# Kernel optimization log

Hardware: AMD Instinct MI355X
Metric: run time of the kernel (lower is better)

The kernel has to match this reference:

```python
import jax, jax.numpy as jnp
import numpy as np

B, D, L, T, K = 16, 256, 256, 1000, 3
DW, DC = 4, 2  # dim_w, dim_c
CH = 8         # ConvSwishBlock out channels (10 = 1 start + 1 end + 8)


def swish(x):
    return x * jax.nn.sigmoid(x)


def setup_inputs() -> dict:
    key = jax.random.key(0)
    ks = jax.random.split(key, 12)
    # durations ~ U[1,6] per phone -> sum ~ 3.5*L ~ 896 <= T
    durations = 1.0 + 5.0 * jax.random.uniform(ks[0], (B, L), dtype=jnp.float32)
    phoneme = jax.random.normal(ks[1], (B, D, L), dtype=jnp.float32)
    # True = padded phone position
    phone_len = L - (jnp.arange(B) % 4) * 16
    phoneme_mask = (jnp.arange(L)[None, :] >= phone_len[:, None])[:, None, :]
    durations = jnp.where(phoneme_mask[:, 0, :], 0.0, durations)
    s = 0.02
    p = {
        'proj_w_W': s * jax.random.normal(ks[2], (D, D)), 'proj_w_b': jnp.zeros((D,)),
        'conv_w_W': s * jax.random.normal(ks[3], (CH, D, K)), 'conv_w_b': jnp.zeros((CH,)),
        'mlp_w_W': s * jax.random.normal(ks[4], (2 + CH, DW)), 'mlp_w_b': jnp.zeros((DW,)),
        'lin_w_W': s * jax.random.normal(ks[5], (D * DW, D)), 'lin_w_b': jnp.zeros((D,)),
        'proj_c_W': s * jax.random.normal(ks[6], (D, D)), 'proj_c_b': jnp.zeros((D,)),
        'conv_c_W': s * jax.random.normal(ks[7], (CH, D, K)), 'conv_c_b': jnp.zeros((CH,)),
        'mlp_c_W': s * jax.random.normal(ks[8], (2 + CH, DC)), 'mlp_c_b': jnp.zeros((DC,)),
        'lin_c_W': s * jax.random.normal(ks[9], (DW * DC, D)), 'lin_c_b': jnp.zeros((D,)),
    }
    return {'durations': durations, 'phoneme': phoneme, 'phoneme_mask': phoneme_mask, **p}


def _conv_branch(x, phone_pad, projW, projb, convW, convb):
    # x: (B, D, L). 1x1 conv projection, then K-wide 'same' conv to CH channels, swish, mask.
    x = jnp.einsum('od,bdl->bol', projW, x) + projb[None, :, None]
    h = jax.lax.conv_general_dilated(x, convW, (1,), 'SAME',
                                     dimension_numbers=('NCH', 'OIH', 'NCH'))
    h = swish(h + convb[None, :, None])
    h = jnp.where(phone_pad[:, None, :], 0.0, h)
    return h.transpose(0, 2, 1)  # (B, L, CH)


def _forward(durations, phoneme, phoneme_mask,
             proj_w_W, proj_w_b, conv_w_W, conv_w_b, mlp_w_W, mlp_w_b, lin_w_W, lin_w_b,
             proj_c_W, proj_c_b, conv_c_W, conv_c_b, mlp_c_W, mlp_c_b, lin_c_W, lin_c_b):
    phone_pad = phoneme_mask[:, 0, :]                       # (B, L) True = pad
    frame_len = jnp.clip(jnp.round(jnp.sum(durations, -1)), 0, T).astype(jnp.int32)
    frame_pad = jnp.arange(T)[None, :] >= frame_len[:, None]  # (B, T) True = pad
    attn_pad = frame_pad[:, :, None] | phone_pad[:, None, :]  # (B, T, L)

    sd = jnp.cumsum(durations, -1)                          # (B, L) cumulative end times
    sk = sd - durations                                     # (B, L) start times
    t = jnp.arange(1, T + 1, dtype=durations.dtype)
    S = jnp.where(attn_pad, 0.0, t[None, :, None] - sk[:, None, :])                    # (B,T,L)
    E = jnp.where(attn_pad, 0.0, jnp.broadcast_to(sd[:, None, :], attn_pad.shape)
                  - sk[:, None, :])                                                    # (B,T,L)

    # W branch: per-(frame, phone) attention weights over phones
    h_w = _conv_branch(phoneme, phone_pad, proj_w_W, proj_w_b, conv_w_W, conv_w_b)     # (B,L,CH)
    feat_w = jnp.concatenate(
        [S[..., None], E[..., None], jnp.broadcast_to(h_w[:, None], (B, T, L, CH))], -1)
    w = swish(feat_w @ mlp_w_W + mlp_w_b)                   # (B, T, L, DW)
    w = jnp.where(phone_pad[:, None, :, None], -jnp.inf, w)
    w = jax.nn.softmax(w, axis=2)                           # softmax over phones
    w = jnp.where(frame_pad[:, :, None, None], 0.0, w)

    # C branch: auxiliary per-(frame, phone) context
    h_c = _conv_branch(phoneme, phone_pad, proj_c_W, proj_c_b, conv_c_W, conv_c_b)
    feat_c = jnp.concatenate(
        [S[..., None], E[..., None], jnp.broadcast_to(h_c[:, None], (B, T, L, CH))], -1)
    c = swish(feat_c @ mlp_c_W + mlp_c_b)                   # (B, T, L, DC)

    # combine: wh = einsum over phones with phoneme features, wc with c matrix
    wh = jnp.einsum('btnq,bnh->btqh', w, phoneme.transpose(0, 2, 1))  # (B,T,DW,D)
    wh = wh.reshape(B, T, DW * D) @ lin_w_W + lin_w_b                 # (B,T,D)
    wc = jnp.einsum('btnq,btnp->btqp', w, c)                          # (B,T,DW,DC)
    wc = wc.reshape(B, T, DW * DC) @ lin_c_W + lin_c_b                # (B,T,D)
    return wh + wc


def reference(durations, phoneme, phoneme_mask,
              proj_w_W, proj_w_b, conv_w_W, conv_w_b, mlp_w_W, mlp_w_b, lin_w_W, lin_w_b,
              proj_c_W, proj_c_b, conv_c_W, conv_c_b, mlp_c_W, mlp_c_b, lin_c_W, lin_c_b):
    return _forward(durations, phoneme, phoneme_mask,
                    proj_w_W, proj_w_b, conv_w_W, conv_w_b, mlp_w_W, mlp_w_b, lin_w_W, lin_w_b,
                    proj_c_W, proj_c_b, conv_c_W, conv_c_b, mlp_c_W, mlp_c_b, lin_c_W, lin_c_b)
```

## Files before the change

### kernel.cpp

```cpp
#include <hip/hip_runtime.h>


typedef short v8s __attribute__((ext_vector_type(8)));
typedef _Float16 v8h __attribute__((ext_vector_type(8)));
typedef float f4 __attribute__((ext_vector_type(4)));

__device__ __forceinline__ float bf2f(unsigned short h) {
  return __uint_as_float(((unsigned int)h) << 16);
}
__device__ __forceinline__ unsigned short f2bf(float f) {
  unsigned int u = __float_as_uint(f);
  u = (u + 0x7FFFu + ((u >> 16) & 1u)) >> 16;
  return (unsigned short)u;
}
__device__ __forceinline__ float swishf(float x) {
  return x * __builtin_amdgcn_rcpf(1.f + __expf(-x));
}

__global__ __launch_bounds__(256) void k_prep(
    const float* __restrict__ dur, const float* __restrict__ ph,
    const float* __restrict__ liWw,
    const float* __restrict__ cvWw, const float* __restrict__ pjWw,
    const float* __restrict__ pjbw,
    const float* __restrict__ cvWc, const float* __restrict__ pjWc,
    const float* __restrict__ pjbc,
    float* __restrict__ sk, int* __restrict__ frame_len,
    unsigned short* __restrict__ Mb, float* __restrict__ bK,
    unsigned short* __restrict__ LWT, unsigned short* __restrict__ phT) {
  __shared__ float sm[32 * 33];
  int blk = blockIdx.x, tid = threadIdx.x;
  if (blk < 16) {
    int b = blk, l = tid;
    float d = dur[b * 256 + l];
    sm[l] = d;
    __syncthreads();
    for (int off = 1; off < 256; off <<= 1) {
      float v = (l >= off) ? sm[l - off] : 0.f;
      __syncthreads();
      sm[l] += v;
      __syncthreads();
    }
    sk[b * 256 + l] = sm[l] - d;
    if (l == 255) {
      int fl = (int)rintf(sm[255]);
      frame_len[b] = min(max(fl, 0), 1000);
    }
  } else if (blk < 64) {
    int x = blk - 16;
    int br = x / 24, ck = x % 24;
    int ch = ck / 3, k = ck % 3;
    const float* convW = br ? cvWc : cvWw;
    const float* projW = br ? pjWc : pjWw;
    const float* projb = br ? pjbc : pjbw;
    int d = tid;
    float a0 = 0.f, a1 = 0.f, a2 = 0.f, a3 = 0.f;
    for (int o = 0; o < 256; o += 4) {
      a0 += convW[ch * 768 + (o + 0) * 3 + k] * projW[(o + 0) * 256 + d];
      a1 += convW[ch * 768 + (o + 1) * 3 + k] * projW[(o + 1) * 256 + d];
      a2 += convW[ch * 768 + (o + 2) * 3 + k] * projW[(o + 2) * 256 + d];
      a3 += convW[ch * 768 + (o + 3) * 3 + k] * projW[(o + 3) * 256 + d];
    }
    Mb[(br * 24 + ck) * 256 + d] = f2bf((a0 + a1) + (a2 + a3));
    if (tid < 64) {
      float pb = 0.f;
      for (int o = tid; o < 256; o += 64)
        pb += convW[ch * 768 + o * 3 + k] * projb[o];
#pragma unroll
      for (int off = 1; off < 64; off <<= 1) pb += __shfl_xor(pb, off);
      if (tid == 0) bK[br * 24 + ck] = pb;
    }
  } else if (blk < 320) {
    int idx = blk - 64;
    int kt = idx & 31, ot = idx >> 5;
    int tx = tid & 31, ty = tid >> 5;
#pragma unroll
    for (int r = 0; r < 4; r++) {
      int row = ty + r * 8;
      sm[row * 33 + tx] = liWw[(size_t)(kt * 32 + row) * 256 + ot * 32 + tx];
    }
    __syncthreads();
#pragma unroll
    for (int r = 0; r < 4; r++) {
      int row = ty + r * 8;
      LWT[(size_t)(ot * 32 + row) * 1024 + kt * 32 + tx] =
          f2bf(sm[tx * 33 + row]);
    }
  } else {
    int idx = blk - 320;
    int ht = idx & 7, lt = (idx >> 3) & 7, b = idx >> 6;
    int tx = tid & 31, ty = tid >> 5;
#pragma unroll
    for (int r = 0; r < 4; r++) {
      int row = ty + r * 8;
      sm[row * 33 + tx] =
          ph[(size_t)b * 65536 + (size_t)(ht * 32 + row) * 256 + lt * 32 + tx];
    }
    __syncthreads();
#pragma unroll
    for (int r = 0; r < 4; r++) {
      int row = ty + r * 8;
      phT[(size_t)b * 65536 + (size_t)(lt * 32 + row) * 256 + ht * 32 + tx] =
          f2bf(sm[tx * 33 + row]);
    }
  }
}

__global__ __launch_bounds__(256) void k_convG(
    const unsigned short* __restrict__ phT, const unsigned short* __restrict__ Mb,
    const float* __restrict__ bK, const float* __restrict__ cvbw,
    const float* __restrict__ cvbc, const float* __restrict__ dur,
    const float* __restrict__ sk, const float* __restrict__ mlpWw,
    const float* __restrict__ mlpbw, const float* __restrict__ mlpWc,
    const float* __restrict__ mlpbc, const unsigned short* __restrict__ LWT,
    float* __restrict__ Lbw, float* __restrict__ Laux,
    float* __restrict__ maxAb, _Float16* __restrict__ G) {
  __shared__ __align__(16) float C[256 * 49];
  __shared__ float redm[4][4];
  int blk = blockIdx.x;
  int tid = threadIdx.x, wave = tid >> 6, lane = tid & 63;
  int quad = lane >> 4, col = lane & 15;
  if (blk < 16) {
    int b = blk;
    int l0 = wave * 64;
    const unsigned short* Ab = phT + (size_t)b * 65536;
    f4 acc[4][3] = {};
#pragma unroll
    for (int k0 = 0; k0 < 256; k0 += 32) {
      v8s af[4], bf[3];
#pragma unroll
      for (int lt = 0; lt < 4; lt++)
        af[lt] = *(const v8s*)(Ab + (size_t)(l0 + lt * 16 + col) * 256 + k0 + quad * 8);
#pragma unroll
      for (int ct = 0; ct < 3; ct++)
        bf[ct] = *(const v8s*)(Mb + (size_t)(ct * 16 + col) * 256 + k0 + quad * 8);
#pragma unroll
      for (int lt = 0; lt < 4; lt++)
#pragma unroll
        for (int ct = 0; ct < 3; ct++)
          acc[lt][ct] = __builtin_amdgcn_mfma_f32_16x16x32_bf16(af[lt], bf[ct],
                                                                acc[lt][ct], 0, 0, 0);
    }
#pragma unroll
    for (int lt = 0; lt < 4; lt++)
#pragma unroll
      for (int ct = 0; ct < 3; ct++)
#pragma unroll
        for (int r = 0; r < 4; r++)
          C[(l0 + lt * 16 + quad * 4 + r) * 49 + ct * 16 + col] = acc[lt][ct][r];
    __syncthreads();
    int l = tid;
    float dv = dur[b * 256 + l];
    bool vld = (dv != 0.f);
    float hv[2][8];
#pragma unroll
    for (int br = 0; br < 2; br++) {
      const float* convb = br ? cvbc : cvbw;
#pragma unroll
      for (int ch = 0; ch < 8; ch++) {
        int ck = br * 24 + ch * 3;
        float v = convb[ch] + bK[ck + 1] + C[l * 49 + ck + 1];
        if (l > 0) v += bK[ck + 0] + C[(l - 1) * 49 + ck + 0];
        if (l < 255) v += bK[ck + 2] + C[(l + 1) * 49 + ck + 2];
        hv[br][ch] = vld ? swishf(v) : 0.f;
      }
    }
    float skl = sk[b * 256 + l];
    float A[4];
#pragma unroll
    for (int q = 0; q < 4; q++) {
      float a = mlpbw[q] + dv * mlpWw[4 + q] - skl * mlpWw[q];
#pragma unroll
      for (int ch = 0; ch < 8; ch++) a += hv[0][ch] * mlpWw[(2 + ch) * 4 + q];
      A[q] = vld ? a : -1e30f;
    }
    float bb0 = mlpbc[0] + dv * mlpWc[2] - skl * mlpWc[0];
    float bb1 = mlpbc[1] + dv * mlpWc[3] - skl * mlpWc[1];
#pragma unroll
    for (int ch = 0; ch < 8; ch++) {
      bb0 += hv[1][ch] * mlpWc[(2 + ch) * 2 + 0];
      bb1 += hv[1][ch] * mlpWc[(2 + ch) * 2 + 1];
    }
    float4 Av = {A[0], A[1], A[2], A[3]};
    ((float4*)Lbw)[b * 256 + l] = Av;
    float4 Xv = {bb0, bb1, vld ? 1.f : 0.f, 0.f};
    ((float4*)Laux)[b * 256 + l] = Xv;
    float m0 = A[0], m1 = A[1], m2 = A[2], m3 = A[3];
#pragma unroll
    for (int off = 1; off < 64; off <<= 1) {
      m0 = fmaxf(m0, __shfl_xor(m0, off));
      m1 = fmaxf(m1, __shfl_xor(m1, off));
      m2 = fmaxf(m2, __shfl_xor(m2, off));
      m3 = fmaxf(m3, __shfl_xor(m3, off));
    }
    if (lane == 0) {
      redm[wave][0] = m0;
      redm[wave][1] = m1;
      redm[wave][2] = m2;
      redm[wave][3] = m3;
    }
    __syncthreads();
    if (tid < 4)
      maxAb[b * 4 + tid] = fmaxf(fmaxf(redm[0][tid], redm[1][tid]),
                                 fmaxf(redm[2][tid], redm[3][tid]));
  } else {
    int idx = blk - 16;
    int b = idx >> 4;
    int sub = idx & 15;
    int q = sub >> 2, quadr = sub & 3;
    int mo = (quadr >> 1) * 128, nl = (quadr & 1) * 128;
    int wm = (wave & 1) * 64, wn = (wave >> 1) * 64;
    const unsigned short* Ag = LWT + (size_t)q * 256;
    const unsigned short* Bg = phT + (size_t)b * 65536;
    f4 acc[4][4] = {};
#pragma unroll
    for (int k0 = 0; k0 < 256; k0 += 32) {
      v8s af[4], bf[4];
#pragma unroll
      for (int mt = 0; mt < 4; mt++)
        af[mt] = *(const v8s*)(Ag + (size_t)(mo + wm + mt * 16 + col) * 1024 +
                               k0 + quad * 8);
#pragma unroll
      for (int nt = 0; nt < 4; nt++)
        bf[nt] = *(const v8s*)(Bg + (size_t)(nl + wn + nt * 16 + col) * 256 +
                               k0 + quad * 8);
#pragma unroll
      for (int mt = 0; mt < 4; mt++)
#pragma unroll
        for (int nt = 0; nt < 4; nt++)
          acc[mt][nt] = __builtin_amdgcn_mfma_f32_16x16x32_bf16(af[mt], bf[nt],
                                                                acc[mt][nt], 0, 0, 0);
    }
    _Float16* Gb = G + (size_t)b * 262144 + q * 256;
#pragma unroll
    for (int mt = 0; mt < 4; mt++)
#pragma unroll
      for (int r = 0; r < 4; r++) {
        int orow = mo + wm + mt * 16 + quad * 4 + r;
#pragma unroll
        for (int nt = 0; nt < 4; nt++) {
          int lcol = nl + wn + nt * 16 + col;
          Gb[(size_t)orow * 1024 + lcol] = (_Float16)acc[mt][nt][r];
        }
      }
  }
}

__global__ __launch_bounds__(256) void k_fuse(
    const float* __restrict__ Lbw, const float* __restrict__ Laux,
    const float* __restrict__ maxAb, const int* __restrict__ frame_len,
    const float* __restrict__ mlpWw, const float* __restrict__ mlpWc,
    const _Float16* __restrict__ G, const float* __restrict__ lwb,
    const float* __restrict__ lcb, const float* __restrict__ LC,
    float* __restrict__ out) {
  __shared__ __align__(16) _Float16 Asm[32 * 512];
  __shared__ __align__(16) float4 Lb4[264];
  __shared__ __align__(16) float4 Lx4[264];
  __shared__ float bias_s[256];
  __shared__ float lcs[8][256];
  __shared__ float wcs[32][8];

  int idx = blockIdx.x;
  int b = (idx & 7) * 2 + ((idx >> 3) & 1);
  int t0 = (idx >> 4) * 32;
  int tid = threadIdx.x, wave = tid >> 6, lane = tid & 63;
  int quad = lane >> 4, col = lane & 15;

  {
    float4 av = ((const float4*)Lbw)[b * 256 + tid];
    float4 xv = ((const float4*)Laux)[b * 256 + tid];
    int li = tid + (tid >> 5);
    Lb4[li] = av;
    Lx4[li] = xv;
    bias_s[tid] = lwb[tid] + lcb[tid];
#pragma unroll
    for (int i = 0; i < 8; i++) lcs[i][tid] = LC[i * 256 + tid];
  }
  int fl = frame_len[b];
  float4 mx4 = ((const float4*)maxAb)[b];
  float mw0 = mlpWw[0], mw1 = mlpWw[1], mw2 = mlpWw[2], mw3 = mlpWw[3];
  float mc0 = mlpWc[0], mc1 = mlpWc[1];

  int r_loc = lane >> 3, l_grp = lane & 7;
  int row = wave * 8 + r_loc;
  int t = t0 + row;
  bool live = (t < fl);
  float tp1 = (float)(t + 1);
  int rsw = row & 7;
  int asw = col & 7;
  int wn = wave * 64;
  f4 acc[2][4] = {};

  __syncthreads();

#pragma unroll
  for (int p = 0; p < 2; ++p) {
    if (p) __syncthreads();
    float mq0 = p ? mw2 : mw0;
    float mq1 = p ? mw3 : mw1;
    float mxa = p ? mx4.z : mx4.x;
    float mxb = p ? mx4.w : mx4.y;
    float m0 = live ? fmaxf(mxa + tp1 * mq0, 0.f) : 1e30f;
    float m1 = live ? fmaxf(mxb + tp1 * mq1, 0.f) : 1e30f;
    float s0 = 0.f, s1 = 0.f, p00 = 0.f, p01 = 0.f, p10 = 0.f, p11 = 0.f;
    v8h e0[4], e1[4];
#pragma unroll
    for (int j = 0; j < 32; ++j) {
      int l = l_grp * 32 + j;
      int li = l + (l >> 5);
      float4 A4 = Lb4[li];
      float4 ax = Lx4[li];
      float cp0 = swishf(ax.x + tp1 * mc0);
      float cp1 = swishf(ax.y + tp1 * mc1);
      float Aq0 = p ? A4.z : A4.x;
      float Aq1 = p ? A4.w : A4.y;
      float ee0 = __expf(swishf(Aq0 + tp1 * mq0) - m0) * ax.z;
      float ee1 = __expf(swishf(Aq1 + tp1 * mq1) - m1) * ax.z;
      e0[j >> 3][j & 7] = (_Float16)ee0;
      e1[j >> 3][j & 7] = (_Float16)ee1;
      s0 += ee0;
      s1 += ee1;
      p00 += ee0 * cp0;
      p01 += ee0 * cp1;
      p10 += ee1 * cp0;
      p11 += ee1 * cp1;
    }
#pragma unroll
    for (int off = 1; off < 8; off <<= 1) {
      s0 += __shfl_xor(s0, off);
      s1 += __shfl_xor(s1, off);
      p00 += __shfl_xor(p00, off);
      p01 += __shfl_xor(p01, off);
      p10 += __shfl_xor(p10, off);
      p11 += __shfl_xor(p11, off);
    }
    float iv0 = live ? __builtin_amdgcn_rcpf(s0) : 0.f;
    float iv1 = live ? __builtin_amdgcn_rcpf(s1) : 0.f;
    if (l_grp == 0) {
      wcs[row][p * 4 + 0] = p00 * iv0;
      wcs[row][p * 4 + 1] = p01 * iv0;
      wcs[row][p * 4 + 2] = p10 * iv1;
      wcs[row][p * 4 + 3] = p11 * iv1;
    }
    _Float16 h0 = (_Float16)iv0, h1 = (_Float16)iv1;
#pragma unroll
    for (int c = 0; c < 4; ++c) {
      int sl0 = (l_grp * 4 + c) ^ rsw;
      int sl1 = 32 + ((l_grp * 4 + c) ^ rsw);
      *(v8h*)&Asm[(row * 64 + sl0) * 8] = e0[c] * h0;
      *(v8h*)&Asm[(row * 64 + sl1) * 8] = e1[c] * h1;
    }
    __syncthreads();
    const _Float16* Gp = G + (size_t)b * 262144 + p * 512;
#pragma unroll 2
    for (int k0 = 0; k0 < 512; k0 += 32) {
      int slk = (k0 >> 3) + quad;
      v8h af0 = *(const v8h*)&Asm[(col * 64 + (slk ^ asw)) * 8];
      v8h af1 = *(const v8h*)&Asm[((16 + col) * 64 + (slk ^ asw)) * 8];
      v8h bf[4];
#pragma unroll
      for (int nt = 0; nt < 4; ++nt)
        bf[nt] =
            *(const v8h*)(Gp + (size_t)(wn + nt * 16 + col) * 1024 + k0 + quad * 8);
#pragma unroll
      for (int nt = 0; nt < 4; ++nt) {
        acc[0][nt] =
            __builtin_amdgcn_mfma_f32_16x16x32_f16(af0, bf[nt], acc[0][nt], 0, 0, 0);
        acc[1][nt] =
            __builtin_amdgcn_mfma_f32_16x16x32_f16(af1, bf[nt], acc[1][nt], 0, 0, 0);
      }
    }
  }
#pragma unroll
  for (int mt = 0; mt < 2; ++mt)
#pragma unroll
    for (int r = 0; r < 4; ++r) {
      int lrow = mt * 16 + quad * 4 + r;
      int trow = t0 + lrow;
      if (trow < 1000) {
        float4 wa = *(const float4*)&wcs[lrow][0];
        float4 wb = *(const float4*)&wcs[lrow][4];
        float wcl[8] = {wa.x, wa.y, wa.z, wa.w, wb.x, wb.y, wb.z, wb.w};
#pragma unroll
        for (int nt = 0; nt < 4; ++nt) {
          int oc = wn + nt * 16 + col;
          float v = acc[mt][nt][r] + bias_s[oc];
#pragma unroll
          for (int jj = 0; jj < 8; ++jj) v = fmaf(wcl[jj], lcs[jj][oc], v);
          out[((size_t)(b * 1000 + trow)) * 256 + oc] = v;
        }
      }
    }
}

extern "C" void kernel_launch(void* const* d_in, const int* in_sizes, int n_in,
                              void* d_out, int out_size, void* d_ws, size_t ws_size,
                              hipStream_t stream) {
  const float* dur  = (const float*)d_in[0];
  const float* ph   = (const float*)d_in[1];
  const float* pjWw = (const float*)d_in[3];
  const float* pjbw = (const float*)d_in[4];
  const float* cvWw = (const float*)d_in[5];
  const float* cvbw = (const float*)d_in[6];
  const float* mlWw = (const float*)d_in[7];
  const float* mlbw = (const float*)d_in[8];
  const float* liWw = (const float*)d_in[9];
  const float* libw = (const float*)d_in[10];
  const float* pjWc = (const float*)d_in[11];
  const float* pjbc = (const float*)d_in[12];
  const float* cvWc = (const float*)d_in[13];
  const float* cvbc = (const float*)d_in[14];
  const float* mlWc = (const float*)d_in[15];
  const float* mlbc = (const float*)d_in[16];
  const float* liWc = (const float*)d_in[17];
  const float* libc = (const float*)d_in[18];
  float* out = (float*)d_out;

  float* f = (float*)d_ws;
  size_t o = 0;
  float* sk = f + o;            o += 4096;
  int* fl = (int*)(f + o);      o += 16;
  float* bK = f + o;            o += 64;
  unsigned short* Mb = (unsigned short*)(f + o); o += 6144;
  float* Lbw = f + o;           o += 16384;
  float* Laux = f + o;          o += 16384;
  float* mxA = f + o;           o += 64;
  _Float16* G = (_Float16*)(f + o);              o += 2097152;
  unsigned short* phT = (unsigned short*)(f + o); o += 524288;
  unsigned short* LWT = (unsigned short*)(f + o); o += 131072;

  k_prep<<<1344, 256, 0, stream>>>(dur, ph, liWw, cvWw, pjWw, pjbw, cvWc, pjWc,
                                   pjbc, sk, fl, Mb, bK, LWT, phT);
  k_convG<<<272, 256, 0, stream>>>(phT, Mb, bK, cvbw, cvbc, dur, sk, mlWw,
                                   mlbw, mlWc, mlbc, LWT, Lbw, Laux, mxA, G);
  k_fuse<<<512, 256, 0, stream>>>(Lbw, Laux, mxA, fl, mlWw, mlWc, G, libw,
                                  libc, liWc, out);
}
```

Before: 175.6 us.

## Double threads per fuse block, split convG tiles finer, skip dead frame tiles

The G-building GEMM in k_convG now uses 64-wide column tiles, which doubles its grid to 528 blocks and halves per-wave accumulators. k_fuse moves to 512 threads per block. Each row is split across 16 lanes instead of 8, the c-branch swish values are computed once instead of per pass, and MFMA priority is raised during the GEMM loop. Blocks whose whole time tile lies beyond the frame length now just write the bias and return, skipping the softmax and GEMM. The trade-offs are more LDS padding and register pressure per thread, and normalisation now uses fp16-rounded exponentials with an exact divide.

```diff
diff --git a/kernel.cpp b/kernel.cpp
--- a/kernel.cpp
+++ b/kernel.cpp
@@ -204,29 +204,29 @@
                                  fmaxf(redm[2][tid], redm[3][tid]));
   } else {
     int idx = blk - 16;
-    int b = idx >> 4;
-    int sub = idx & 15;
-    int q = sub >> 2, quadr = sub & 3;
-    int mo = (quadr >> 1) * 128, nl = (quadr & 1) * 128;
-    int wm = (wave & 1) * 64, wn = (wave >> 1) * 64;
+    int b = idx >> 5;
+    int sub = idx & 31;
+    int q = sub >> 3, rem = sub & 7;
+    int mo = (rem >> 2) * 128, nl = (rem & 3) * 64;
+    int wm = (wave & 1) * 64, wn = (wave >> 1) * 32;
     const unsigned short* Ag = LWT + (size_t)q * 256;
     const unsigned short* Bg = phT + (size_t)b * 65536;
-    f4 acc[4][4] = {};
+    f4 acc[4][2] = {};
 #pragma unroll
     for (int k0 = 0; k0 < 256; k0 += 32) {
-      v8s af[4], bf[4];
+      v8s af[4], bf[2];
 #pragma unroll
       for (int mt = 0; mt < 4; mt++)
         af[mt] = *(const v8s*)(Ag + (size_t)(mo + wm + mt * 16 + col) * 1024 +
                                k0 + quad * 8);
 #pragma unroll
-      for (int nt = 0; nt < 4; nt++)
+      for (int nt = 0; nt < 2; nt++)
         bf[nt] = *(const v8s*)(Bg + (size_t)(nl + wn + nt * 16 + col) * 256 +
                                k0 + quad * 8);
 #pragma unroll
       for (int mt = 0; mt < 4; mt++)
 #pragma unroll
-        for (int nt = 0; nt < 4; nt++)
+        for (int nt = 0; nt < 2; nt++)
           acc[mt][nt] = __builtin_amdgcn_mfma_f32_16x16x32_bf16(af[mt], bf[nt],
                                                                 acc[mt][nt], 0, 0, 0);
     }
@@ -237,7 +237,7 @@
       for (int r = 0; r < 4; r++) {
         int orow = mo + wm + mt * 16 + quad * 4 + r;
 #pragma unroll
-        for (int nt = 0; nt < 4; nt++) {
+        for (int nt = 0; nt < 2; nt++) {
           int lcol = nl + wn + nt * 16 + col;
           Gb[(size_t)orow * 1024 + lcol] = (_Float16)acc[mt][nt][r];
         }
@@ -245,7 +245,7 @@
   }
 }
 
-__global__ __launch_bounds__(256) void k_fuse(
+__global__ __launch_bounds__(512, 4) void k_fuse(
     const float* __restrict__ Lbw, const float* __restrict__ Laux,
     const float* __restrict__ maxAb, const int* __restrict__ frame_len,
     const float* __restrict__ mlpWw, const float* __restrict__ mlpWc,
@@ -253,8 +253,8 @@
     const float* __restrict__ lcb, const float* __restrict__ LC,
     float* __restrict__ out) {
   __shared__ __align__(16) _Float16 Asm[32 * 512];
-  __shared__ __align__(16) float4 Lb4[264];
-  __shared__ __align__(16) float4 Lx4[264];
+  __shared__ __align__(16) float4 Lb4[272];
+  __shared__ __align__(16) float4 Lx4[272];
   __shared__ float bias_s[256];
   __shared__ float lcs[8][256];
   __shared__ float wcs[32][8];
@@ -265,32 +265,52 @@
   int tid = threadIdx.x, wave = tid >> 6, lane = tid & 63;
   int quad = lane >> 4, col = lane & 15;
 
-  {
+  int fl = frame_len[b];
+  if (t0 >= fl) {
+    int o = tid & 255;
+    float v = lwb[o] + lcb[o];
+    for (int r = tid >> 8; r < 32; r += 2) {
+      int t = t0 + r;
+      if (t < 1000) out[((size_t)(b * 1000 + t)) * 256 + o] = v;
+    }
+    return;
+  }
+
+  if (tid < 256) {
     float4 av = ((const float4*)Lbw)[b * 256 + tid];
     float4 xv = ((const float4*)Laux)[b * 256 + tid];
-    int li = tid + (tid >> 5);
+    int li = tid + (tid >> 4);
     Lb4[li] = av;
     Lx4[li] = xv;
     bias_s[tid] = lwb[tid] + lcb[tid];
-#pragma unroll
-    for (int i = 0; i < 8; i++) lcs[i][tid] = LC[i * 256 + tid];
-  }
-  int fl = frame_len[b];
+  }
+  for (int i = tid; i < 2048; i += 512) lcs[i >> 8][i & 255] = LC[i];
+
   float4 mx4 = ((const float4*)maxAb)[b];
   float mw0 = mlpWw[0], mw1 = mlpWw[1], mw2 = mlpWw[2], mw3 = mlpWw[3];
   float mc0 = mlpWc[0], mc1 = mlpWc[1];
 
-  int r_loc = lane >> 3, l_grp = lane & 7;
-  int row = wave * 8 + r_loc;
+  int l_grp = lane & 15;
+  int row = wave * 4 + (lane >> 4);
   int t = t0 + row;
   bool live = (t < fl);
   float tp1 = (float)(t + 1);
   int rsw = row & 7;
   int asw = col & 7;
-  int wn = wave * 64;
-  f4 acc[2][4] = {};
+  int wn = wave * 32;
+  f4 acc[2][2] = {};
 
   __syncthreads();
+
+  float cpa[16], cpb[16];
+#pragma unroll
+  for (int j = 0; j < 16; ++j) {
+    int l = l_grp * 16 + j;
+    int li = l + (l >> 4);
+    float4 ax = Lx4[li];
+    cpa[j] = swishf(ax.x + tp1 * mc0);
+    cpb[j] = swishf(ax.y + tp1 * mc1);
+  }
 
 #pragma unroll
   for (int p = 0; p < 2; ++p) {
@@ -302,30 +322,29 @@
     float m0 = live ? fmaxf(mxa + tp1 * mq0, 0.f) : 1e30f;
     float m1 = live ? fmaxf(mxb + tp1 * mq1, 0.f) : 1e30f;
     float s0 = 0.f, s1 = 0.f, p00 = 0.f, p01 = 0.f, p10 = 0.f, p11 = 0.f;
-    v8h e0[4], e1[4];
-#pragma unroll
-    for (int j = 0; j < 32; ++j) {
-      int l = l_grp * 32 + j;
-      int li = l + (l >> 5);
+    v8h e0[2], e1[2];
+#pragma unroll
+    for (int j = 0; j < 16; ++j) {
+      int l = l_grp * 16 + j;
+      int li = l + (l >> 4);
       float4 A4 = Lb4[li];
-      float4 ax = Lx4[li];
-      float cp0 = swishf(ax.x + tp1 * mc0);
-      float cp1 = swishf(ax.y + tp1 * mc1);
+      float zz = ((const float*)&Lx4[li])[2];
       float Aq0 = p ? A4.z : A4.x;
       float Aq1 = p ? A4.w : A4.y;
-      float ee0 = __expf(swishf(Aq0 + tp1 * mq0) - m0) * ax.z;
-      float ee1 = __expf(swishf(Aq1 + tp1 * mq1) - m1) * ax.z;
-      e0[j >> 3][j & 7] = (_Float16)ee0;
-      e1[j >> 3][j & 7] = (_Float16)ee1;
-      s0 += ee0;
-      s1 += ee1;
-      p00 += ee0 * cp0;
-      p01 += ee0 * cp1;
-      p10 += ee1 * cp0;
-      p11 += ee1 * cp1;
-    }
-#pragma unroll
-    for (int off = 1; off < 8; off <<= 1) {
+      _Float16 eh0 = (_Float16)(__expf(swishf(Aq0 + tp1 * mq0) - m0) * zz);
+      _Float16 eh1 = (_Float16)(__expf(swishf(Aq1 + tp1 * mq1) - m1) * zz);
+      e0[j >> 3][j & 7] = eh0;
+      e1[j >> 3][j & 7] = eh1;
+      float f0 = (float)eh0, f1 = (float)eh1;
+      s0 += f0;
+      s1 += f1;
+      p00 += f0 * cpa[j];
+      p01 += f0 * cpb[j];
+      p10 += f1 * cpa[j];
+      p11 += f1 * cpb[j];
+    }
+#pragma unroll
+    for (int off = 1; off < 16; off <<= 1) {
       s0 += __shfl_xor(s0, off);
       s1 += __shfl_xor(s1, off);
       p00 += __shfl_xor(p00, off);
@@ -333,42 +352,48 @@
       p10 += __shfl_xor(p10, off);
       p11 += __shfl_xor(p11, off);
     }
-    float iv0 = live ? __builtin_amdgcn_rcpf(s0) : 0.f;
-    float iv1 = live ? __builtin_amdgcn_rcpf(s1) : 0.f;
+    float iv0 = live ? 1.0f / s0 : 0.f;
+    float iv1 = live ? 1.0f / s1 : 0.f;
     if (l_grp == 0) {
       wcs[row][p * 4 + 0] = p00 * iv0;
       wcs[row][p * 4 + 1] = p01 * iv0;
       wcs[row][p * 4 + 2] = p10 * iv1;
       wcs[row][p * 4 + 3] = p11 * iv1;
     }
-    _Float16 h0 = (_Float16)iv0, h1 = (_Float16)iv1;
-#pragma unroll
-    for (int c = 0; c < 4; ++c) {
-      int sl0 = (l_grp * 4 + c) ^ rsw;
-      int sl1 = 32 + ((l_grp * 4 + c) ^ rsw);
-      *(v8h*)&Asm[(row * 64 + sl0) * 8] = e0[c] * h0;
-      *(v8h*)&Asm[(row * 64 + sl1) * 8] = e1[c] * h1;
+#pragma unroll
+    for (int c = 0; c < 2; ++c) {
+      int sl = (l_grp * 2 + c) ^ rsw;
+      v8h w0, w1;
+#pragma unroll
+      for (int k = 0; k < 8; ++k) {
+        w0[k] = (_Float16)((float)e0[c][k] * iv0);
+        w1[k] = (_Float16)((float)e1[c][k] * iv1);
+      }
+      *(v8h*)&Asm[(row * 64 + sl) * 8] = w0;
+      *(v8h*)&Asm[(row * 64 + 32 + sl) * 8] = w1;
     }
     __syncthreads();
     const _Float16* Gp = G + (size_t)b * 262144 + p * 512;
+    __builtin_amdgcn_s_setprio(1);
 #pragma unroll 2
     for (int k0 = 0; k0 < 512; k0 += 32) {
       int slk = (k0 >> 3) + quad;
-      v8h af0 = *(const v8h*)&Asm[(col * 64 + (slk ^ asw)) * 8];
-      v8h af1 = *(const v8h*)&Asm[((16 + col) * 64 + (slk ^ asw)) * 8];
-      v8h bf[4];
-#pragma unroll
-      for (int nt = 0; nt < 4; ++nt)
+      v8h af[2], bf[2];
+#pragma unroll
+      for (int mt = 0; mt < 2; ++mt)
+        af[mt] = *(const v8h*)&Asm[((mt * 16 + col) * 64 + (slk ^ asw)) * 8];
+#pragma unroll
+      for (int nt = 0; nt < 2; ++nt)
         bf[nt] =
             *(const v8h*)(Gp + (size_t)(wn + nt * 16 + col) * 1024 + k0 + quad * 8);
 #pragma unroll
-      for (int nt = 0; nt < 4; ++nt) {
-        acc[0][nt] =
-            __builtin_amdgcn_mfma_f32_16x16x32_f16(af0, bf[nt], acc[0][nt], 0, 0, 0);
-        acc[1][nt] =
-            __builtin_amdgcn_mfma_f32_16x16x32_f16(af1, bf[nt], acc[1][nt], 0, 0, 0);
-      }
-    }
+      for (int mt = 0; mt < 2; ++mt)
+#pragma unroll
+        for (int nt = 0; nt < 2; ++nt)
+          acc[mt][nt] = __builtin_amdgcn_mfma_f32_16x16x32_f16(af[mt], bf[nt],
+                                                               acc[mt][nt], 0, 0, 0);
+    }
+    __builtin_amdgcn_s_setprio(0);
   }
 #pragma unroll
   for (int mt = 0; mt < 2; ++mt)
@@ -381,7 +406,7 @@
         float4 wb = *(const float4*)&wcs[lrow][4];
         float wcl[8] = {wa.x, wa.y, wa.z, wa.w, wb.x, wb.y, wb.z, wb.w};
 #pragma unroll
-        for (int nt = 0; nt < 4; ++nt) {
+        for (int nt = 0; nt < 2; ++nt) {
           int oc = wn + nt * 16 + col;
           float v = acc[mt][nt][r] + bias_s[oc];
 #pragma unroll
@@ -430,8 +455,8 @@
 
   k_prep<<<1344, 256, 0, stream>>>(dur, ph, liWw, cvWw, pjWw, pjbw, cvWc, pjWc,
                                    pjbc, sk, fl, Mb, bK, LWT, phT);
-  k_convG<<<272, 256, 0, stream>>>(phT, Mb, bK, cvbw, cvbc, dur, sk, mlWw,
+  k_convG<<<528, 256, 0, stream>>>(phT, Mb, bK, cvbw, cvbc, dur, sk, mlWw,
                                    mlbw, mlWc, mlbc, LWT, Lbw, Laux, mxA, G);
-  k_fuse<<<512, 256, 0, stream>>>(Lbw, Laux, mxA, fl, mlWw, mlWc, G, libw,
+  k_fuse<<<512, 512, 0, stream>>>(Lbw, Laux, mxA, fl, mlWw, mlWc, G, libw,
                                   libc, liWc, out);
 }
```

Result: no change. 177.8 us (+1.2%).
